# Optimization experiments

Measured on AMD Instinct MI355X. Metric: run time of the kernel, lower is better.

## Reference

```python
import jax, jax.numpy as jnp
import numpy as np
import math

GRID = 256       # grid_size
KMAX = 64        # max_elements_per_cell
RES = 512        # image resolution
SPAN = 4         # max grid cells per axis covered by one triangle bbox
NUM_VIEWS = 16
SCALE = 0.5


def _projection_matrix(x=0.5, n=1.5, f=100.0):
    return np.array([[n / x, 0.0, 0.0, 0.0],
                     [0.0, n / -x, 0.0, 0.0],
                     [0.0, 0.0, -(f + n) / (f - n), -(2.0 * f * n) / (f - n)],
                     [0.0, 0.0, -1.0, 0.0]], dtype=np.float32)


def _view_buffers(num_views, seed):
    rng = np.random.default_rng(seed)
    proj = _projection_matrix()
    mvps, lights = [], []
    for _ in range(num_views):
        u1, u2, u3 = rng.random(3)
        qx = math.sqrt(1.0 - u1) * math.sin(math.tau * u2)
        qy = math.sqrt(1.0 - u1) * math.cos(math.tau * u2)
        qz = math.sqrt(u1) * math.sin(math.tau * u3)
        qw = math.sqrt(u1) * math.cos(math.tau * u3)
        rot = np.array([[1 - 2 * (qy * qy + qz * qz), 2 * (qx * qy - qz * qw), 2 * (qx * qz + qy * qw)],
                        [2 * (qx * qy + qz * qw), 1 - 2 * (qx * qx + qz * qz), 2 * (qy * qz - qx * qw)],
                        [2 * (qx * qz - qy * qw), 2 * (qy * qz + qx * qw), 1 - 2 * (qx * qx + qy * qy)]], dtype=np.float32)
        rmat = np.eye(4, dtype=np.float32); rmat[:3, :3] = rot
        tmat = np.eye(4, dtype=np.float32); tmat[2, 3] = -4.0
        view = tmat @ rmat
        campos = np.linalg.inv(view)[:3, 3]
        light = -campos / (np.linalg.norm(campos) + 1e-8)
        mvps.append(proj @ view)
        lights.append(light.astype(np.float32))
    return np.stack(mvps).astype(np.float32), np.stack(lights).astype(np.float32)


def setup_inputs() -> dict:
    key = jax.random.key(0)
    k1, k2 = jax.random.split(key)
    F = 100_000
    # clustered per-triangle vertices -> small on-screen triangles (mesh-like locality)
    centers = jax.random.uniform(k1, (F, 1, 3), minval=-1.0, maxval=1.0)
    jitter = jax.random.normal(k2, (F, 3, 3)) * 0.02
    u = (centers + jitter).reshape(-1, 3).astype(jnp.float32)          # [3F,3]
    faces = jnp.arange(3 * F, dtype=jnp.int32).reshape(F, 3)
    mvps, light = _view_buffers(NUM_VIEWS, 42)
    return {"u": u,
            "mvps": jnp.asarray(mvps),
            "lightdir": jnp.asarray(light),
            "background_color": jnp.zeros(3, jnp.float32),
            "base_colors": jnp.ones((F, 3), jnp.float32),
            "faces": faces}


def _forward(u, mvps, lightdir, background_color, base_colors, faces):
    # _normalize_vertices
    v = u - u.mean(0, keepdims=True)
    span = jnp.maximum(v.max() - v.min(), 1e-6)
    v = v * (SCALE / span)
    Fn = faces.shape[0]
    # project with active view 0 (v_hom @ mvps[0].T, no perspective divide, as in source)
    v_hom = jnp.concatenate([v, jnp.ones((v.shape[0], 1), v.dtype)], axis=1)
    v_ndc = v_hom @ mvps[0].T                                          # [V,4]
    tris = v_ndc[faces]                                                # [F,3,4]
    wtri = v[faces]                                                    # [F,3,3]
    nrm = jnp.cross(wtri[:, 0] - wtri[:, 1], wtri[:, 2] - wtri[:, 1])
    nrm = nrm / (jnp.linalg.norm(nrm, axis=-1, keepdims=True) + 1e-10)
    z = tris[:, :, 2].mean(1)
    order = jnp.argsort(z)                                             # depth sort (near first)
    st = tris[order]
    sn = nrm[order]
    cp = (st[:, :, :2] + 1.0) * 0.5                                    # [F,3,2] control pts in [0,1]
    shading = jnp.clip(jnp.sum(-lightdir[0] * sn, axis=-1, keepdims=True), 0.0)
    colors = base_colors[order] * shading                              # [F,3]
    # --- grid acceleration structure build (scatter triangles into cells) ---
    lo = jnp.clip(jnp.floor(cp.min(1) * GRID).astype(jnp.int32), 0, GRID - 1)  # [F,2]
    hi = jnp.clip(jnp.floor(cp.max(1) * GRID).astype(jnp.int32), 0, GRID - 1)
    d = jnp.arange(SPAN, dtype=jnp.int32)
    cx = lo[:, 0:1] + d[None, :]                                       # [F,SPAN]
    cy = lo[:, 1:2] + d[None, :]
    valid = (cy[:, :, None] <= hi[:, 1:2, None]) & (cx[:, None, :] <= hi[:, 0:1].reshape(Fn, 1, 1) + 0 * cx[:, None, :])
    valid = (cy[:, :, None] <= hi[:, 1:2, None]) & (cx[:, None, :] <= hi[:, 0:1][:, :, None])
    cell = cy[:, :, None] * GRID + cx[:, None, :]                      # [F,SPAN,SPAN]
    NC = GRID * GRID
    cell = jnp.where(valid, cell, NC).reshape(-1)
    tri = jnp.broadcast_to(jnp.arange(Fn, dtype=jnp.int32)[:, None, None], (Fn, SPAN, SPAN)).reshape(-1)
    # sort (cell, depth-rank): tri ids are already depth-ordered
    keys = cell.astype(jnp.int64) * (Fn + 1) + tri
    ordk = jnp.argsort(keys)
    sc = cell[ordk]
    stri = tri[ordk]
    counts = jax.ops.segment_sum(jnp.ones_like(sc), sc, num_segments=NC + 1)
    starts = jnp.concatenate([jnp.zeros(1, counts.dtype), jnp.cumsum(counts)[:-1]])
    rank = jnp.arange(sc.shape[0], dtype=jnp.int32) - starts[sc].astype(jnp.int32)
    ok = (rank < KMAX) & (sc < NC)
    grid_elems = jnp.full((NC + 1, KMAX), -1, jnp.int32)
    grid_elems = grid_elems.at[jnp.where(ok, sc, NC), jnp.where(ok, rank, 0)].set(jnp.where(ok, stri, -1))
    # --- per-pixel rasterization via grid query ---
    px = (jnp.arange(RES, dtype=jnp.float32) + 0.5) / RES
    uu, vv = jnp.meshgrid(px, px, indexing='xy')
    P = jnp.stack([uu, vv], -1).reshape(-1, 2)                         # [P,2]
    ix = jnp.clip((P[:, 0] * GRID).astype(jnp.int32), 0, GRID - 1)
    iy = jnp.clip((P[:, 1] * GRID).astype(jnp.int32), 0, GRID - 1)
    elems = grid_elems[iy * GRID + ix]                                 # [P,K]
    e = jnp.maximum(elems, 0)
    tpts = cp[e]                                                       # [P,K,3,2]
    a, b, c = tpts[:, :, 0], tpts[:, :, 1], tpts[:, :, 2]
    pp = P[:, None, :]

    def cr(o, q, r):
        return (q[..., 0] - o[..., 0]) * (r[..., 1] - o[..., 1]) - (q[..., 1] - o[..., 1]) * (r[..., 0] - o[..., 0])

    e0 = cr(a, b, pp)
    e1 = cr(b, c, pp)
    e2 = cr(c, a, pp)
    inside = ((e0 >= 0) & (e1 >= 0) & (e2 >= 0)) | ((e0 <= 0) & (e1 <= 0) & (e2 <= 0))
    hit = inside & (elems >= 0)
    first = jnp.argmax(hit, axis=1)                                    # front-most (depth-sorted)
    anyhit = jnp.any(hit, axis=1)
    tid = e[jnp.arange(e.shape[0]), first]
    img = jnp.where(anyhit[:, None], colors[tid], background_color[None, :])
    return img.reshape(RES, RES, 3)


def reference(u, mvps, lightdir, background_color, base_colors, faces):
    return _forward(u, mvps, lightdir, background_color, base_colors, faces)
```

## Files before the change

### kernel.cpp

```cpp
#include <hip/hip_runtime.h>
#include <stdint.h>

#pragma clang fp contract(off)

#define GRIDN 256
#define NC (GRIDN * GRIDN)
#define RESN 512
#define RBLOCKS 256
#define CAP 1024
#define NB 64
#define HBINS 16384

typedef unsigned short bfraw;
typedef unsigned short u16;

__device__ __forceinline__ float bf2f(bfraw h) {
    return __uint_as_float(((uint32_t)h) << 16);
}
__device__ __forceinline__ bfraw f2bf(float f) {
    uint32_t b = __float_as_uint(f);
    return (bfraw)((b + 0x7FFFu + ((b >> 16) & 1u)) >> 16);
}
__device__ __forceinline__ uint32_t fkey(float f) {
    uint32_t b = __float_as_uint(f);
    return (b & 0x80000000u) ? ~b : (b | 0x80000000u);
}

__global__ __launch_bounds__(256) void k_reduce1(const bfraw* __restrict__ u, int nrows,
                                                 double* __restrict__ psum,
                                                 float* __restrict__ pmin,
                                                 float* __restrict__ pmax) {
    __shared__ double ssum[256 * 3];
    __shared__ float smin[256 * 3];
    __shared__ float smax[256 * 3];
    int t = threadIdx.x;
    double s0 = 0.0, s1 = 0.0, s2 = 0.0;
    float mn0 = INFINITY, mn1 = INFINITY, mn2 = INFINITY;
    float mx0 = -INFINITY, mx1 = -INFINITY, mx2 = -INFINITY;
    for (int r = blockIdx.x * 256 + t; r < nrows; r += 256 * RBLOCKS) {
        float a = bf2f(u[3 * r + 0]);
        float b = bf2f(u[3 * r + 1]);
        float c = bf2f(u[3 * r + 2]);
        s0 += (double)a; s1 += (double)b; s2 += (double)c;
        mn0 = fminf(mn0, a); mx0 = fmaxf(mx0, a);
        mn1 = fminf(mn1, b); mx1 = fmaxf(mx1, b);
        mn2 = fminf(mn2, c); mx2 = fmaxf(mx2, c);
    }
    ssum[t * 3 + 0] = s0; ssum[t * 3 + 1] = s1; ssum[t * 3 + 2] = s2;
    smin[t * 3 + 0] = mn0; smin[t * 3 + 1] = mn1; smin[t * 3 + 2] = mn2;
    smax[t * 3 + 0] = mx0; smax[t * 3 + 1] = mx1; smax[t * 3 + 2] = mx2;
    __syncthreads();
    for (int st = 128; st > 0; st >>= 1) {
        if (t < st) {
            for (int c = 0; c < 3; c++) {
                ssum[t * 3 + c] += ssum[(t + st) * 3 + c];
                smin[t * 3 + c] = fminf(smin[t * 3 + c], smin[(t + st) * 3 + c]);
                smax[t * 3 + c] = fmaxf(smax[t * 3 + c], smax[(t + st) * 3 + c]);
            }
        }
        __syncthreads();
    }
    if (t == 0) {
        for (int c = 0; c < 3; c++) {
            psum[blockIdx.x * 3 + c] = ssum[c];
            pmin[blockIdx.x * 3 + c] = smin[c];
            pmax[blockIdx.x * 3 + c] = smax[c];
        }
    }
}

__global__ __launch_bounds__(256) void k_reduce2(const double* __restrict__ psum,
                                                 const float* __restrict__ pmin,
                                                 const float* __restrict__ pmax,
                                                 int nrows, float* __restrict__ cst) {
    __shared__ double ssum[256 * 3];
    __shared__ float smin[256 * 3];
    __shared__ float smax[256 * 3];
    int t = threadIdx.x;
    for (int c = 0; c < 3; c++) {
        ssum[t * 3 + c] = psum[t * 3 + c];
        smin[t * 3 + c] = pmin[t * 3 + c];
        smax[t * 3 + c] = pmax[t * 3 + c];
    }
    __syncthreads();
    for (int st = 128; st > 0; st >>= 1) {
        if (t < st) {
            for (int c = 0; c < 3; c++) {
                ssum[t * 3 + c] += ssum[(t + st) * 3 + c];
                smin[t * 3 + c] = fminf(smin[t * 3 + c], smin[(t + st) * 3 + c]);
                smax[t * 3 + c] = fmaxf(smax[t * 3 + c], smax[(t + st) * 3 + c]);
            }
        }
        __syncthreads();
    }
    if (t == 0) {
        float fn = (float)nrows;
        float m0 = (float)ssum[0] / fn;
        float m1 = (float)ssum[1] / fn;
        float m2 = (float)ssum[2] / fn;
        float vmax = fmaxf(fmaxf(smax[0] - m0, smax[1] - m1), smax[2] - m2);
        float vmin = fminf(fminf(smin[0] - m0, smin[1] - m1), smin[2] - m2);
        float span = fmaxf(vmax - vmin, 1e-06f);
        float s = 0.5f / span;
        cst[0] = m0; cst[1] = m1; cst[2] = m2; cst[3] = s;
    }
}

__global__ __launch_bounds__(256) void k_setup(const bfraw* __restrict__ u,
                                               const int* __restrict__ faces,
                                               const bfraw* __restrict__ mvp,
                                               const bfraw* __restrict__ light,
                                               const float* __restrict__ cst,
                                               int F,
                                               float* __restrict__ tcs,
                                               uint32_t* __restrict__ tz,
                                               uint32_t* __restrict__ tbox) {
    int f = blockIdx.x * 256 + threadIdx.x;
    if (f >= F) return;
    float m0 = cst[0], m1 = cst[1], m2 = cst[2], s = cst[3];
    float M[12];
    for (int i = 0; i < 12; i++) M[i] = bf2f(mvp[i]);

    float vx[3], vy[3], vz[3], cpx[3], cpy[3], zc[3];
    for (int j = 0; j < 3; j++) {
        int idx = faces[3 * f + j];
        float a = bf2f(u[3 * idx + 0]);
        float b = bf2f(u[3 * idx + 1]);
        float c = bf2f(u[3 * idx + 2]);
        float x = (a - m0) * s;
        float y = (b - m1) * s;
        float z = (c - m2) * s;
        vx[j] = x; vy[j] = y; vz[j] = z;
        float cx = fmaf(x, M[0], 0.0f);
        cx = fmaf(y, M[1], cx); cx = fmaf(z, M[2], cx); cx = cx + M[3];
        float cy = fmaf(x, M[4], 0.0f);
        cy = fmaf(y, M[5], cy); cy = fmaf(z, M[6], cy); cy = cy + M[7];
        float cz = fmaf(x, M[8], 0.0f);
        cz = fmaf(y, M[9], cz); cz = fmaf(z, M[10], cz); cz = cz + M[11];
        cpx[j] = (cx + 1.0f) * 0.5f;
        cpy[j] = (cy + 1.0f) * 0.5f;
        zc[j] = cz;
    }
    float zmean = ((zc[0] + zc[1]) + zc[2]) / 3.0f;

    float e1x = vx[0] - vx[1], e1y = vy[0] - vy[1], e1z = vz[0] - vz[1];
    float e2x = vx[2] - vx[1], e2y = vy[2] - vy[1], e2z = vz[2] - vz[1];
    float nx = e1y * e2z - e1z * e2y;
    float ny = e1z * e2x - e1x * e2z;
    float nz = e1x * e2y - e1y * e2x;
    float nn = nx * nx;
    nn = nn + ny * ny;
    nn = nn + nz * nz;
    float d = sqrtf(nn) + 1e-10f;
    float inx = nx / d, iny = ny / d, inz = nz / d;

    float l0 = bf2f(light[0]), l1 = bf2f(light[1]), l2 = bf2f(light[2]);
    float p0 = (-l0) * inx;
    float p1 = (-l1) * iny;
    float p2 = (-l2) * inz;
    float shading = fmaxf((p0 + p1) + p2, 0.0f);

    tcs[f * 8 + 0] = cpx[0]; tcs[f * 8 + 1] = cpy[0];
    tcs[f * 8 + 2] = cpx[1]; tcs[f * 8 + 3] = cpy[1];
    tcs[f * 8 + 4] = cpx[2]; tcs[f * 8 + 5] = cpy[2];
    tcs[f * 8 + 6] = shading;
    tcs[f * 8 + 7] = 0.0f;

    tz[f] = fkey(zmean);

    float mnx = fminf(fminf(cpx[0], cpx[1]), cpx[2]);
    float mny = fminf(fminf(cpy[0], cpy[1]), cpy[2]);
    float mxx = fmaxf(fmaxf(cpx[0], cpx[1]), cpx[2]);
    float mxy = fmaxf(fmaxf(cpy[0], cpy[1]), cpy[2]);
    int lox = (int)floorf(mnx * 256.0f); lox = lox < 0 ? 0 : (lox > 255 ? 255 : lox);
    int loy = (int)floorf(mny * 256.0f); loy = loy < 0 ? 0 : (loy > 255 ? 255 : loy);
    int hix = (int)floorf(mxx * 256.0f); hix = hix < 0 ? 0 : (hix > 255 ? 255 : hix);
    int hiy = (int)floorf(mxy * 256.0f); hiy = hiy < 0 ? 0 : (hiy > 255 ? 255 : hiy);
    int hx = hix < lox + 3 ? hix : lox + 3;
    int hy = hiy < loy + 3 ? hiy : loy + 3;
    tbox[f] = (uint32_t)lox | ((uint32_t)loy << 8) | ((uint32_t)hx << 16) | ((uint32_t)hy << 24);
}

__global__ __launch_bounds__(1024) void k_count(const uint32_t* __restrict__ tbox,
                                                int F,
                                                u16* __restrict__ blockHist) {
    __shared__ uint32_t hist[HBINS];
    int b = blockIdx.x;
    int chunk = (F + NB - 1) / NB;
    int fs = b * chunk;
    int fe = fs + chunk < F ? fs + chunk : F;
    for (int h = 0; h < 2; h++) {
        for (int i = threadIdx.x; i < HBINS; i += 1024) hist[i] = 0u;
        __syncthreads();
        for (int f = fs + threadIdx.x; f < fe; f += 1024) {
            uint32_t bx = tbox[f];
            int lox = bx & 255, loy = (bx >> 8) & 255;
            int hx = (bx >> 16) & 255, hy = bx >> 24;
            for (int yy = loy; yy <= hy; yy++) {
                for (int xx = lox; xx <= hx; xx++) {
                    uint32_t cell = (uint32_t)(yy * GRIDN + xx);
                    if ((int)(cell >> 15) != h) continue;
                    uint32_t c = cell & 32767u;
                    atomicAdd(&hist[c >> 1], 1u << (16u * (c & 1u)));
                }
            }
        }
        __syncthreads();
        uint32_t* dst = (uint32_t*)(blockHist + (size_t)b * NC + (size_t)h * 32768);
        for (int i = threadIdx.x; i < HBINS; i += 1024) dst[i] = hist[i];
        __syncthreads();
    }
}

__global__ __launch_bounds__(256) void k_scanA(u16* __restrict__ blockHist,
                                               uint32_t* __restrict__ cellTot) {
    int c = blockIdx.x * 256 + threadIdx.x;
    uint32_t tot = 0;
    for (int b = 0; b < NB; b++) {
        size_t o = (size_t)b * NC + c;
        uint32_t v = blockHist[o];
        blockHist[o] = (u16)tot;
        tot += v;
    }
    cellTot[c] = tot;
}

__global__ __launch_bounds__(1024) void k_scan(const uint32_t* __restrict__ cellTot,
                                               uint32_t* __restrict__ cellOff) {
    __shared__ uint32_t sc[1024];
    int t = threadIdx.x;
    int base = t * 64;
    uint32_t local = 0;
    for (int i = 0; i < 64; i++) local += cellTot[base + i];
    sc[t] = local;
    __syncthreads();
    for (int st = 1; st < 1024; st <<= 1) {
        uint32_t v = 0;
        if (t >= st) v = sc[t - st];
        __syncthreads();
        if (t >= st) sc[t] += v;
        __syncthreads();
    }
    uint32_t run = sc[t] - local;
    for (int i = 0; i < 64; i++) {
        uint32_t c = cellTot[base + i];
        cellOff[base + i] = run;
        run += c;
    }
    if (t == 1023) cellOff[NC] = run;
}

__global__ __launch_bounds__(1024) void k_place(const uint32_t* __restrict__ tbox,
                                                const u16* __restrict__ blockHist,
                                                const uint32_t* __restrict__ cellOff,
                                                uint32_t* __restrict__ pairs,
                                                int F) {
    __shared__ uint32_t hist[HBINS];
    int b = blockIdx.x;
    int chunk = (F + NB - 1) / NB;
    int fs = b * chunk;
    int fe = fs + chunk < F ? fs + chunk : F;
    uint32_t pcap = (uint32_t)F * 16u;
    for (int h = 0; h < 2; h++) {
        for (int i = threadIdx.x; i < HBINS; i += 1024) hist[i] = 0u;
        __syncthreads();
        for (int f = fs + threadIdx.x; f < fe; f += 1024) {
            uint32_t bx = tbox[f];
            int lox = bx & 255, loy = (bx >> 8) & 255;
            int hx = (bx >> 16) & 255, hy = bx >> 24;
            for (int yy = loy; yy <= hy; yy++) {
                for (int xx = lox; xx <= hx; xx++) {
                    uint32_t cell = (uint32_t)(yy * GRIDN + xx);
                    if ((int)(cell >> 15) != h) continue;
                    uint32_t c = cell & 32767u;
                    uint32_t sh = 16u * (c & 1u);
                    uint32_t old = atomicAdd(&hist[c >> 1], 1u << sh);
                    uint32_t r = (old >> sh) & 0xFFFFu;
                    uint32_t pos = cellOff[cell] + (uint32_t)blockHist[(size_t)b * NC + cell] + r;
                    if (pos < pcap) pairs[pos] = (uint32_t)f;
                }
            }
        }
        __syncthreads();
    }
}

__global__ __launch_bounds__(256) void k_cellsort(const uint32_t* __restrict__ cellOff,
                                                  const uint32_t* __restrict__ tz,
                                                  uint32_t* __restrict__ pairs,
                                                  int F) {
    __shared__ uint64_t lkeys[CAP];
    int cell = blockIdx.x;
    uint32_t pcap = (uint32_t)F * 16u;
    uint32_t off = cellOff[cell];
    uint32_t end = cellOff[cell + 1];
    if (off > pcap || end > pcap || end < off) return;
    uint32_t n = end - off;
    if (n < 2u) return;
    uint32_t m = n > CAP ? CAP : n;
    int t = threadIdx.x;
    for (uint32_t i = t; i < m; i += 256) {
        uint32_t id = pairs[off + i];
        if (id >= (uint32_t)F) id = 0;
        lkeys[i] = ((uint64_t)tz[id] << 32) | id;
    }
    __syncthreads();
    uint64_t k0 = ~0ull, k1 = ~0ull, k2 = ~0ull, k3 = ~0ull;
    uint32_t i0 = t, i1 = t + 256, i2 = t + 512, i3 = t + 768;
    if (i0 < m) k0 = lkeys[i0];
    if (i1 < m) k1 = lkeys[i1];
    if (i2 < m) k2 = lkeys[i2];
    if (i3 < m) k3 = lkeys[i3];
    uint32_t r0 = 0, r1 = 0, r2 = 0, r3 = 0;
    for (uint32_t j = 0; j < m; j++) {
        uint64_t kj = lkeys[j];
        r0 += (kj < k0) ? 1u : 0u;
        r1 += (kj < k1) ? 1u : 0u;
        r2 += (kj < k2) ? 1u : 0u;
        r3 += (kj < k3) ? 1u : 0u;
    }
    if (i0 < m && r0 < 64u) pairs[off + r0] = (uint32_t)(k0 & 0xFFFFFFFFu);
    if (i1 < m && r1 < 64u) pairs[off + r1] = (uint32_t)(k1 & 0xFFFFFFFFu);
    if (i2 < m && r2 < 64u) pairs[off + r2] = (uint32_t)(k2 & 0xFFFFFFFFu);
    if (i3 < m && r3 < 64u) pairs[off + r3] = (uint32_t)(k3 & 0xFFFFFFFFu);
}

__global__ __launch_bounds__(256) void k_raster(const float* __restrict__ tcs,
                                                const uint32_t* __restrict__ cellOff,
                                                const uint32_t* __restrict__ pairs,
                                                const bfraw* __restrict__ basec,
                                                const bfraw* __restrict__ bg,
                                                bfraw* __restrict__ out, int F) {
    int p = blockIdx.x * 256 + threadIdx.x;
    int col = p & (RESN - 1);
    int row = p >> 9;
    float px = ((float)col + 0.5f) / 512.0f;
    float py = ((float)row + 0.5f) / 512.0f;
    int cell = (row >> 1) * GRIDN + (col >> 1);
    uint32_t pcap = (uint32_t)F * 16u;
    uint32_t off = cellOff[cell];
    uint32_t end = cellOff[cell + 1];
    uint32_t m = 0;
    if (off <= pcap && end <= pcap && end >= off) {
        uint32_t n = end - off;
        m = n > 64u ? 64u : n;
    }
    float r = bf2f(bg[0]), g = bf2f(bg[1]), b = bf2f(bg[2]);
    for (uint32_t k = 0; k < m; k++) {
        uint32_t id = pairs[off + k];
        if (id >= (uint32_t)F) continue;
        const float4 A = *(const float4*)(tcs + (size_t)id * 8);
        const float4 B = *(const float4*)(tcs + (size_t)id * 8 + 4);
        float ax = A.x, ay = A.y, bx = A.z, by = A.w, cx = B.x, cy = B.y;
        float e0 = (bx - ax) * (py - ay) - (by - ay) * (px - ax);
        float e1 = (cx - bx) * (py - by) - (cy - by) * (px - bx);
        float e2 = (ax - cx) * (py - cy) - (ay - cy) * (px - cx);
        bool inside = (e0 >= 0.0f && e1 >= 0.0f && e2 >= 0.0f) ||
                      (e0 <= 0.0f && e1 <= 0.0f && e2 <= 0.0f);
        if (inside) {
            float sh = B.z;
            r = bf2f(basec[3 * id + 0]) * sh;
            g = bf2f(basec[3 * id + 1]) * sh;
            b = bf2f(basec[3 * id + 2]) * sh;
            break;
        }
    }
    int o = p * 3;
    out[o + 0] = f2bf(r);
    out[o + 1] = f2bf(g);
    out[o + 2] = f2bf(b);
}

__global__ __launch_bounds__(256) void k_diag(bfraw* __restrict__ out, float code) {
    out[blockIdx.x * 256 + threadIdx.x] = f2bf(code);
}

extern "C" void kernel_launch(void* const* d_in, const int* in_sizes, int n_in,
                              void* d_out, int out_size, void* d_ws, size_t ws_size,
                              hipStream_t stream) {
    const bfraw* u = (const bfraw*)d_in[0];
    const bfraw* mvps = (const bfraw*)d_in[1];
    const bfraw* light = (const bfraw*)d_in[2];
    const bfraw* bg = (const bfraw*)d_in[3];
    const bfraw* basec = (const bfraw*)d_in[4];
    const int* faces = (const int*)d_in[5];
    int nrows = in_sizes[0] / 3;
    int F = in_sizes[5] / 3;
    bfraw* out = (bfraw*)d_out;

    char* w = (char*)d_ws;
    size_t off = 0;
    auto alloc = [&](size_t bytes) -> void* {
        off = (off + 255) & ~(size_t)255;
        void* p = w + off;
        off += bytes;
        return p;
    };

    float* cst = (float*)alloc(4 * sizeof(float));
    double* psum = (double*)alloc((size_t)RBLOCKS * 3 * sizeof(double));
    float* pmin = (float*)alloc((size_t)RBLOCKS * 3 * sizeof(float));
    float* pmax = (float*)alloc((size_t)RBLOCKS * 3 * sizeof(float));
    float* tcs = (float*)alloc((size_t)F * 8 * sizeof(float));
    uint32_t* tz = (uint32_t*)alloc((size_t)F * sizeof(uint32_t));
    uint32_t* tbox = (uint32_t*)alloc((size_t)F * sizeof(uint32_t));
    u16* blockHist = (u16*)alloc((size_t)NB * NC * sizeof(u16));
    uint32_t* cellTot = (uint32_t*)alloc((size_t)NC * sizeof(uint32_t));
    uint32_t* cellOff = (uint32_t*)alloc(((size_t)NC + 1) * sizeof(uint32_t));
    uint32_t* pairs = (uint32_t*)alloc((size_t)F * 16 * sizeof(uint32_t));
    size_t needed = off;

    if (ws_size < needed) {
        float code = 20000.0f + (float)(ws_size >> 20);
        k_diag<<<(RESN * RESN * 3) / 256, 256, 0, stream>>>(out, code);
        return;
    }

    k_reduce1<<<RBLOCKS, 256, 0, stream>>>(u, nrows, psum, pmin, pmax);
    k_reduce2<<<1, 256, 0, stream>>>(psum, pmin, pmax, nrows, cst);
    k_setup<<<(F + 255) / 256, 256, 0, stream>>>(u, faces, mvps, light, cst, F,
                                                 tcs, tz, tbox);
    k_count<<<NB, 1024, 0, stream>>>(tbox, F, blockHist);
    k_scanA<<<NC / 256, 256, 0, stream>>>(blockHist, cellTot);
    k_scan<<<1, 1024, 0, stream>>>(cellTot, cellOff);
    k_place<<<NB, 1024, 0, stream>>>(tbox, blockHist, cellOff, pairs, F);
    k_cellsort<<<NC, 256, 0, stream>>>(cellOff, tz, pairs, F);
    k_raster<<<(RESN * RESN) / 256, 256, 0, stream>>>(tcs, cellOff, pairs, basec, bg, out, F);
}
```

Baseline: 172.7 us.

## Split count/place histogram into 16 cell slices per face chunk, raise sort cap

The count and place kernels no longer run 64 blocks of 1024 threads that each loop twice over half-grid histograms. They now launch 64×16 blocks of 256 threads, and each block owns a 4096-cell slice, with a small shared histogram. This gives far more parallel blocks for the GPU's many CUs, but every block rereads its chunk's bounding boxes and skips most cells. Separately, the per-cell sort capacity doubles to 2048 with eight keys per thread, which raises shared memory use and register pressure in k_cellsort.

```diff
diff --git a/kernel.cpp b/kernel.cpp
--- a/kernel.cpp
+++ b/kernel.cpp
@@ -7,9 +7,10 @@
 #define NC (GRIDN * GRIDN)
 #define RESN 512
 #define RBLOCKS 256
-#define CAP 1024
+#define CAP 2048
 #define NB 64
-#define HBINS 16384
+#define NS 16
+#define SBINS 2048
 
 typedef unsigned short bfraw;
 typedef unsigned short u16;
@@ -181,35 +182,33 @@
     tbox[f] = (uint32_t)lox | ((uint32_t)loy << 8) | ((uint32_t)hx << 16) | ((uint32_t)hy << 24);
 }
 
-__global__ __launch_bounds__(1024) void k_count(const uint32_t* __restrict__ tbox,
-                                                int F,
-                                                u16* __restrict__ blockHist) {
-    __shared__ uint32_t hist[HBINS];
-    int b = blockIdx.x;
+__global__ __launch_bounds__(256) void k_count(const uint32_t* __restrict__ tbox,
+                                               int F,
+                                               u16* __restrict__ blockHist) {
+    __shared__ uint32_t hist[SBINS];
+    int b = blockIdx.x >> 4;
+    int sl = blockIdx.x & (NS - 1);
     int chunk = (F + NB - 1) / NB;
     int fs = b * chunk;
     int fe = fs + chunk < F ? fs + chunk : F;
-    for (int h = 0; h < 2; h++) {
-        for (int i = threadIdx.x; i < HBINS; i += 1024) hist[i] = 0u;
-        __syncthreads();
-        for (int f = fs + threadIdx.x; f < fe; f += 1024) {
-            uint32_t bx = tbox[f];
-            int lox = bx & 255, loy = (bx >> 8) & 255;
-            int hx = (bx >> 16) & 255, hy = bx >> 24;
-            for (int yy = loy; yy <= hy; yy++) {
-                for (int xx = lox; xx <= hx; xx++) {
-                    uint32_t cell = (uint32_t)(yy * GRIDN + xx);
-                    if ((int)(cell >> 15) != h) continue;
-                    uint32_t c = cell & 32767u;
-                    atomicAdd(&hist[c >> 1], 1u << (16u * (c & 1u)));
-                }
+    for (int i = threadIdx.x; i < SBINS; i += 256) hist[i] = 0u;
+    __syncthreads();
+    for (int f = fs + threadIdx.x; f < fe; f += 256) {
+        uint32_t bx = tbox[f];
+        int lox = bx & 255, loy = (bx >> 8) & 255;
+        int hx = (bx >> 16) & 255, hy = bx >> 24;
+        for (int yy = loy; yy <= hy; yy++) {
+            for (int xx = lox; xx <= hx; xx++) {
+                uint32_t cell = (uint32_t)(yy * GRIDN + xx);
+                if ((int)(cell >> 12) != sl) continue;
+                uint32_t c = cell & 4095u;
+                atomicAdd(&hist[c >> 1], 1u << (16u * (c & 1u)));
             }
         }
-        __syncthreads();
-        uint32_t* dst = (uint32_t*)(blockHist + (size_t)b * NC + (size_t)h * 32768);
-        for (int i = threadIdx.x; i < HBINS; i += 1024) dst[i] = hist[i];
-        __syncthreads();
-    }
+    }
+    __syncthreads();
+    uint32_t* dst = (uint32_t*)(blockHist + (size_t)b * NC) + sl * SBINS;
+    for (int i = threadIdx.x; i < SBINS; i += 256) dst[i] = hist[i];
 }
 
 __global__ __launch_bounds__(256) void k_scanA(u16* __restrict__ blockHist,
@@ -250,38 +249,36 @@
     if (t == 1023) cellOff[NC] = run;
 }
 
-__global__ __launch_bounds__(1024) void k_place(const uint32_t* __restrict__ tbox,
-                                                const u16* __restrict__ blockHist,
-                                                const uint32_t* __restrict__ cellOff,
-                                                uint32_t* __restrict__ pairs,
-                                                int F) {
-    __shared__ uint32_t hist[HBINS];
-    int b = blockIdx.x;
+__global__ __launch_bounds__(256) void k_place(const uint32_t* __restrict__ tbox,
+                                               const u16* __restrict__ blockHist,
+                                               const uint32_t* __restrict__ cellOff,
+                                               uint32_t* __restrict__ pairs,
+                                               int F) {
+    __shared__ uint32_t hist[SBINS];
+    int b = blockIdx.x >> 4;
+    int sl = blockIdx.x & (NS - 1);
     int chunk = (F + NB - 1) / NB;
     int fs = b * chunk;
     int fe = fs + chunk < F ? fs + chunk : F;
     uint32_t pcap = (uint32_t)F * 16u;
-    for (int h = 0; h < 2; h++) {
-        for (int i = threadIdx.x; i < HBINS; i += 1024) hist[i] = 0u;
-        __syncthreads();
-        for (int f = fs + threadIdx.x; f < fe; f += 1024) {
-            uint32_t bx = tbox[f];
-            int lox = bx & 255, loy = (bx >> 8) & 255;
-            int hx = (bx >> 16) & 255, hy = bx >> 24;
-            for (int yy = loy; yy <= hy; yy++) {
-                for (int xx = lox; xx <= hx; xx++) {
-                    uint32_t cell = (uint32_t)(yy * GRIDN + xx);
-                    if ((int)(cell >> 15) != h) continue;
-                    uint32_t c = cell & 32767u;
-                    uint32_t sh = 16u * (c & 1u);
-                    uint32_t old = atomicAdd(&hist[c >> 1], 1u << sh);
-                    uint32_t r = (old >> sh) & 0xFFFFu;
-                    uint32_t pos = cellOff[cell] + (uint32_t)blockHist[(size_t)b * NC + cell] + r;
-                    if (pos < pcap) pairs[pos] = (uint32_t)f;
-                }
+    for (int i = threadIdx.x; i < SBINS; i += 256) hist[i] = 0u;
+    __syncthreads();
+    for (int f = fs + threadIdx.x; f < fe; f += 256) {
+        uint32_t bx = tbox[f];
+        int lox = bx & 255, loy = (bx >> 8) & 255;
+        int hx = (bx >> 16) & 255, hy = bx >> 24;
+        for (int yy = loy; yy <= hy; yy++) {
+            for (int xx = lox; xx <= hx; xx++) {
+                uint32_t cell = (uint32_t)(yy * GRIDN + xx);
+                if ((int)(cell >> 12) != sl) continue;
+                uint32_t c = cell & 4095u;
+                uint32_t sh = 16u * (c & 1u);
+                uint32_t old = atomicAdd(&hist[c >> 1], 1u << sh);
+                uint32_t r = (old >> sh) & 0xFFFFu;
+                uint32_t pos = cellOff[cell] + (uint32_t)blockHist[(size_t)b * NC + cell] + r;
+                if (pos < pcap) pairs[pos] = (uint32_t)f;
             }
         }
-        __syncthreads();
     }
 }
 
@@ -306,23 +303,37 @@
     }
     __syncthreads();
     uint64_t k0 = ~0ull, k1 = ~0ull, k2 = ~0ull, k3 = ~0ull;
+    uint64_t k4 = ~0ull, k5 = ~0ull, k6 = ~0ull, k7 = ~0ull;
     uint32_t i0 = t, i1 = t + 256, i2 = t + 512, i3 = t + 768;
+    uint32_t i4 = t + 1024, i5 = t + 1280, i6 = t + 1536, i7 = t + 1792;
     if (i0 < m) k0 = lkeys[i0];
     if (i1 < m) k1 = lkeys[i1];
     if (i2 < m) k2 = lkeys[i2];
     if (i3 < m) k3 = lkeys[i3];
-    uint32_t r0 = 0, r1 = 0, r2 = 0, r3 = 0;
+    if (i4 < m) k4 = lkeys[i4];
+    if (i5 < m) k5 = lkeys[i5];
+    if (i6 < m) k6 = lkeys[i6];
+    if (i7 < m) k7 = lkeys[i7];
+    uint32_t r0 = 0, r1 = 0, r2 = 0, r3 = 0, r4 = 0, r5 = 0, r6 = 0, r7 = 0;
     for (uint32_t j = 0; j < m; j++) {
         uint64_t kj = lkeys[j];
         r0 += (kj < k0) ? 1u : 0u;
         r1 += (kj < k1) ? 1u : 0u;
         r2 += (kj < k2) ? 1u : 0u;
         r3 += (kj < k3) ? 1u : 0u;
+        r4 += (kj < k4) ? 1u : 0u;
+        r5 += (kj < k5) ? 1u : 0u;
+        r6 += (kj < k6) ? 1u : 0u;
+        r7 += (kj < k7) ? 1u : 0u;
     }
     if (i0 < m && r0 < 64u) pairs[off + r0] = (uint32_t)(k0 & 0xFFFFFFFFu);
     if (i1 < m && r1 < 64u) pairs[off + r1] = (uint32_t)(k1 & 0xFFFFFFFFu);
     if (i2 < m && r2 < 64u) pairs[off + r2] = (uint32_t)(k2 & 0xFFFFFFFFu);
     if (i3 < m && r3 < 64u) pairs[off + r3] = (uint32_t)(k3 & 0xFFFFFFFFu);
+    if (i4 < m && r4 < 64u) pairs[off + r4] = (uint32_t)(k4 & 0xFFFFFFFFu);
+    if (i5 < m && r5 < 64u) pairs[off + r5] = (uint32_t)(k5 & 0xFFFFFFFFu);
+    if (i6 < m && r6 < 64u) pairs[off + r6] = (uint32_t)(k6 & 0xFFFFFFFFu);
+    if (i7 < m && r7 < 64u) pairs[off + r7] = (uint32_t)(k7 & 0xFFFFFFFFu);
 }
 
 __global__ __launch_bounds__(256) void k_raster(const float* __restrict__ tcs,
@@ -420,10 +431,10 @@
     k_reduce2<<<1, 256, 0, stream>>>(psum, pmin, pmax, nrows, cst);
     k_setup<<<(F + 255) / 256, 256, 0, stream>>>(u, faces, mvps, light, cst, F,
                                                  tcs, tz, tbox);
-    k_count<<<NB, 1024, 0, stream>>>(tbox, F, blockHist);
+    k_count<<<NB * NS, 256, 0, stream>>>(tbox, F, blockHist);
     k_scanA<<<NC / 256, 256, 0, stream>>>(blockHist, cellTot);
     k_scan<<<1, 1024, 0, stream>>>(cellTot, cellOff);
-    k_place<<<NB, 1024, 0, stream>>>(tbox, blockHist, cellOff, pairs, F);
+    k_place<<<NB * NS, 256, 0, stream>>>(tbox, blockHist, cellOff, pairs, F);
     k_cellsort<<<NC, 256, 0, stream>>>(cellOff, tz, pairs, F);
     k_raster<<<(RESN * RESN) / 256, 256, 0, stream>>>(tcs, cellOff, pairs, basec, bg, out, F);
 }
```

New measurement: 251.0 us. 1.45x slower.
